# Kernel tuning notes

Measured on AMD Instinct MI355X. Metric: run time of the kernel, lower is better.

## Reference

```python
import jax, jax.numpy as jnp
import numpy as np

B, L, H = 256, 16, 512
D2 = 2 * H  # bidirectional tree-LSTM hidden dim


def setup_inputs() -> dict:
    key = jax.random.key(0)
    ks = jax.random.split(key, 8)
    sc = lambda k, shp, fan: (jax.random.normal(k, shp, jnp.float32) / np.sqrt(fan)).astype(jnp.float32)
    return {
        "idiom_hidden": jax.random.normal(ks[0], (B, L, H), jnp.float32),
        "idiom_length": jax.random.randint(ks[1], (B,), 2, L + 1, jnp.int32),
        "w_ih_f": sc(ks[2], (4 * H, H), H),
        "w_hh_f": sc(ks[3], (4 * H, H), H),
        "b_f": jnp.zeros((4 * H,), jnp.float32),   # b_ih + b_hh fused
        "w_ih_b": sc(ks[4], (4 * H, H), H),
        "w_hh_b": sc(ks[5], (4 * H, H), H),
        "b_b": jnp.zeros((4 * H,), jnp.float32),
        "w_comp": sc(ks[6], (5 * D2, 2 * D2), 2 * D2),
        "b_comp": jnp.zeros((5 * D2,), jnp.float32),
        "w_query": sc(ks[7], (1, D2), D2),
    }


def _lstm(x, w_ih, w_hh, b):
    # x: (B, T, H) -> hs, cs: (B, T, H). PyTorch LSTMCell gate order: i, f, g, o.
    xg = jnp.einsum("bth,gh->btg", x, w_ih) + b  # precompute input gates

    def step(carry, xg_t):
        h, c = carry
        g = xg_t + h @ w_hh.T
        i, f, u, o = jnp.split(g, 4, axis=-1)
        c = jax.nn.sigmoid(f) * c + jax.nn.sigmoid(i) * jnp.tanh(u)
        h = jax.nn.sigmoid(o) * jnp.tanh(c)
        return (h, c), (h, c)

    z = jnp.zeros((x.shape[0], w_hh.shape[1]), x.dtype)
    _, (hs, cs) = jax.lax.scan(step, (z, z), jnp.swapaxes(xg, 0, 1))
    return jnp.swapaxes(hs, 0, 1), jnp.swapaxes(cs, 0, 1)


def _reverse_padded(x, lengths):
    # reverse first `length` positions of each sequence (batch_first)
    T = x.shape[1]
    pos = jnp.arange(T)[None, :]
    ln = lengths[:, None]
    idx = jnp.where(pos < ln, ln - 1 - pos, pos)
    return jnp.take_along_axis(x, idx[:, :, None], axis=1)


def _treelstm(hl, cl, hr, cr, w, b):
    v = jnp.concatenate([hl, hr], axis=-1) @ w.T + b
    i, fl, fr, u, o = jnp.split(v, 5, axis=-1)
    c = cl * jax.nn.sigmoid(fl + 1.0) + cr * jax.nn.sigmoid(fr + 1.0) + jnp.tanh(u) * jax.nn.sigmoid(i)
    h = jax.nn.sigmoid(o) * jnp.tanh(c)
    return h, c


def reference(idiom_hidden, idiom_length, w_ih_f, w_hh_f, b_f, w_ih_b, w_hh_b, b_b, w_comp, b_comp, w_query):
    maxd = idiom_hidden.shape[1]
    lmask = (jnp.arange(maxd)[None, :] < idiom_length[:, None]).astype(idiom_hidden.dtype)

    # bidirectional leaf LSTM
    hs_f, cs_f = _lstm(idiom_hidden, w_ih_f, w_hh_f, b_f)
    x_bw = _reverse_padded(idiom_hidden, idiom_length)
    hs_b, cs_b = _lstm(x_bw, w_ih_b, w_hh_b, b_b)
    hs_b = _reverse_padded(hs_b, idiom_length)
    cs_b = _reverse_padded(cs_b, idiom_length)
    h = jnp.concatenate([hs_f, hs_b], axis=-1)  # (B, L, 2H)
    c = jnp.concatenate([cs_f, cs_b], axis=-1)

    # iterative tree-LSTM composition (shapes shrink by 1 each step -> Python loop over depth)
    for i in range(maxd - 1):
        hl, hr = h[:, :-1, :], h[:, 1:, :]
        cl, cr = c[:, :-1, :], c[:, 1:, :]
        nh, nc = _treelstm(hl, cl, hr, cr, w_comp, b_comp)
        if i < maxd - 2:
            logits = jnp.einsum("bmd,d->bm", nh, w_query[0])
            m = lmask[:, i + 1:]
            masked = logits + (1.0 - m) * -10000.0  # eval-mode greedy_select
            sel = jax.lax.stop_gradient(
                jax.nn.one_hot(jnp.argmax(masked, axis=1), masked.shape[1], dtype=nh.dtype))
            cum = jnp.cumsum(sel, axis=1)
            left = (1.0 - cum)[:, :, None]
            right = (cum - sel)[:, :, None]
            nh = sel[:, :, None] * nh + left * hl + right * hr
            nc = sel[:, :, None] * nc + left * cl + right * cr
        done = lmask[:, i + 1][:, None, None]
        h = done * nh + (1.0 - done) * h[:, :-1, :]
        c = done * nc + (1.0 - done) * c[:, :-1, :]
    # state collapsed to a single node
    return h[:, 0, :]
```

## Files before the change

### kernel.cpp

```cpp
#include <hip/hip_runtime.h>
#include <math.h>

#define NB 256
#define LM 16
#define HID 512
#define H4 2048
#define D2 1024
#define D5 5120
#define NPAIR0 3840
#define INC_CAP 512

typedef __attribute__((ext_vector_type(8))) short bf16x8;
typedef __attribute__((ext_vector_type(4))) float f32x4;

__device__ __forceinline__ float sigm(float x) { return 1.0f / (1.0f + expf(-x)); }

__device__ __forceinline__ unsigned short bf16_rne(float f) {
    union { float f; unsigned u; } v; v.f = f;
    unsigned u = v.u;
    return (unsigned short)((u + 0x7fffu + ((u >> 16) & 1u)) >> 16);
}
__device__ __forceinline__ float bf16_tof(unsigned short h) {
    union { unsigned u; float f; } v; v.u = ((unsigned)h) << 16;
    return v.f;
}

__device__ __forceinline__ void gload16(const unsigned short* g, unsigned short* l) {
    __builtin_amdgcn_global_load_lds(
        (const __attribute__((address_space(1))) void*)(const void*)g,
        (__attribute__((address_space(3))) void*)(void*)l, 16, 0, 0);
}

__global__ __launch_bounds__(256)
void init_kernel(const int* __restrict__ lens, float* ccur,
                 unsigned short* hc_hi, unsigned short* hc_lo,
                 int* pos, int* pair, int4* rowlist0, int4* rowlist_c,
                 int* rcount, float* logits)
{
    int b = blockIdx.x, tid = threadIdx.x;
    for (int u = tid; u < HID; u += 256) {
        ccur[(size_t)b * HID + u] = 0.f;
        ccur[((size_t)NB + b) * HID + u] = 0.f;
        hc_hi[(size_t)b * HID + u] = 0;
        hc_hi[((size_t)NB + b) * HID + u] = 0;
        hc_lo[(size_t)b * HID + u] = 0;
        hc_lo[((size_t)NB + b) * HID + u] = 0;
    }
    if (tid < 16) { pos[b * 16 + tid] = tid; pair[b * 16 + tid] = tid; logits[b * 16 + tid] = -1e30f; }
    if (tid < 15) rowlist0[b * 15 + tid] = make_int4(b, tid, tid + 1, tid | (tid << 16));
    __shared__ int sbase;
    int len = lens[b];
    if (tid == 0) sbase = atomicAdd(rcount + 15, len - 1);
    __syncthreads();
    if (tid < len - 1) rowlist_c[sbase + tid] = make_int4(b, tid, tid + 1, tid | (tid << 16));
}

__global__ __launch_bounds__(256)
void split_w(const float4* __restrict__ w, unsigned short* __restrict__ hi,
             unsigned short* __restrict__ lo, int n4)
{
    for (int i = blockIdx.x * 256 + threadIdx.x; i < n4; i += gridDim.x * 256) {
        float4 f = w[i];
        ushort4 h, l;
        h.x = bf16_rne(f.x); l.x = bf16_rne(f.x - bf16_tof(h.x));
        h.y = bf16_rne(f.y); l.y = bf16_rne(f.y - bf16_tof(h.y));
        h.z = bf16_rne(f.z); l.z = bf16_rne(f.z - bf16_tof(h.z));
        h.w = bf16_rne(f.w); l.w = bf16_rne(f.w - bf16_tof(h.w));
        ((ushort4*)hi)[i] = h;
        ((ushort4*)lo)[i] = l;
    }
}

__global__ __launch_bounds__(256)
void pack_lstm_w(const float* __restrict__ w_ih_f, const float* __restrict__ w_hh_f,
                 const float* __restrict__ w_ih_b, const float* __restrict__ w_hh_b,
                 unsigned short* __restrict__ wl_hi, unsigned short* __restrict__ wl_lo)
{
    const int total4 = 2 * H4 * 256;
    for (int i = blockIdx.x * 256 + threadIdx.x; i < total4; i += gridDim.x * 256) {
        int k4 = i & 255;
        int j = (i >> 8) & 2047;
        int dir = i >> 19;
        const float* wih = dir ? w_ih_b : w_ih_f;
        const float* whh = dir ? w_hh_b : w_hh_f;
        float4 f = (k4 < 128) ? *(const float4*)(wih + (size_t)j * HID + k4 * 4)
                              : *(const float4*)(whh + (size_t)j * HID + (k4 - 128) * 4);
        ushort4 h, l;
        h.x = bf16_rne(f.x); l.x = bf16_rne(f.x - bf16_tof(h.x));
        h.y = bf16_rne(f.y); l.y = bf16_rne(f.y - bf16_tof(h.y));
        h.z = bf16_rne(f.z); l.z = bf16_rne(f.z - bf16_tof(h.z));
        h.w = bf16_rne(f.w); l.w = bf16_rne(f.w - bf16_tof(h.w));
        ((ushort4*)wl_hi)[i] = h;
        ((ushort4*)wl_lo)[i] = l;
    }
}

__global__ __launch_bounds__(256)
void gemm_lstm_g(int t, const int* __restrict__ lens,
                 const unsigned short* __restrict__ x_hi, const unsigned short* __restrict__ x_lo,
                 const unsigned short* __restrict__ hc_hi, const unsigned short* __restrict__ hc_lo,
                 const unsigned short* __restrict__ wl_hi, const unsigned short* __restrict__ wl_lo,
                 float* __restrict__ gbuf)
{
    constexpr int SA = 64 * 32;
    constexpr int SB = 128 * 32;
    constexpr int BUF = 2 * SA + 2 * SB;

    const int row0 = blockIdx.x * 64;
    const int col0 = blockIdx.y * 128;
    const int dir = blockIdx.z & 1;
    const int kz = blockIdx.z >> 1;
    const int kbeg = kz * 512, kend = kbeg + 512;
    float* gout = gbuf + (size_t)kz * 2 * NB * H4;

    const int tid = threadIdx.x, lane = tid & 63, w = tid >> 6;
    const int wm = w >> 1, wn = w & 1;

    __shared__ __align__(16) unsigned short smem[2 * BUF];

    const int sz8 = ((lane & 3) ^ ((lane >> 3) & 3)) * 8;
    const int b0 = row0 + w * 16 + (lane >> 2);
    const int len = lens[b0];
    const int trow = dir ? ((t < len) ? (len - 1 - t) : t) : t;
    const size_t xoff = ((size_t)(b0 * LM + trow)) * HID;
    const size_t hoff = ((size_t)(dir * NB + b0)) * HID;

    size_t colOff[2];
#pragma unroll
    for (int cs = 0; cs < 2; ++cs)
        colOff[cs] = ((size_t)(dir * H4 + col0 + (w + 4 * cs) * 16 + (lane >> 2))) * 1024;

    auto stage = [&](int d, int k) {
        unsigned short* sb = smem + d * BUF;
        const unsigned short* sh = (k < HID) ? (x_hi + xoff + k) : (hc_hi + hoff + (k - HID));
        gload16(sh + sz8, sb + w * 512);
        const unsigned short* sl = (k < HID) ? (x_lo + xoff + k) : (hc_lo + hoff + (k - HID));
        gload16(sl + sz8, sb + SA + w * 512);
#pragma unroll
        for (int j = 0; j < 4; ++j) {
            const int pl = j >> 1, cs = j & 1;
            const unsigned short* wb = pl ? wl_lo : wl_hi;
            gload16(wb + colOff[cs] + k + sz8, sb + 2 * SA + pl * SB + (w + 4 * cs) * 512);
        }
    };

    f32x4 acc[2][4];
#pragma unroll
    for (int i = 0; i < 2; ++i)
#pragma unroll
        for (int j = 0; j < 4; ++j) acc[i][j] = (f32x4){0.f, 0.f, 0.f, 0.f};

    const int rsw = ((lane >> 4) ^ ((lane >> 1) & 3)) * 8;
    const int a_off = (wm * 32 + (lane & 15)) * 32 + rsw;
    const int b_off = 2 * SA + (wn * 64 + (lane & 15)) * 32 + rsw;

    stage(0, kbeg);
    __syncthreads();
    int cur = 0;
    for (int k0 = kbeg; k0 < kend; k0 += 32) {
        if (k0 + 32 < kend) stage(cur ^ 1, k0 + 32);
        const unsigned short* sb = smem + cur * BUF;
        bf16x8 ah[2], al[2];
#pragma unroll
        for (int fm = 0; fm < 2; ++fm) {
            ah[fm] = *(const bf16x8*)&sb[a_off + fm * 512];
            al[fm] = *(const bf16x8*)&sb[SA + a_off + fm * 512];
        }
#pragma unroll
        for (int fn = 0; fn < 4; ++fn) {
            bf16x8 bh = *(const bf16x8*)&sb[b_off + fn * 512];
            bf16x8 bl = *(const bf16x8*)&sb[SB + b_off + fn * 512];
#pragma unroll
            for (int fm = 0; fm < 2; ++fm) {
                acc[fm][fn] = __builtin_amdgcn_mfma_f32_16x16x32_bf16(ah[fm], bh, acc[fm][fn], 0, 0, 0);
                acc[fm][fn] = __builtin_amdgcn_mfma_f32_16x16x32_bf16(ah[fm], bl, acc[fm][fn], 0, 0, 0);
                acc[fm][fn] = __builtin_amdgcn_mfma_f32_16x16x32_bf16(al[fm], bh, acc[fm][fn], 0, 0, 0);
            }
        }
        __syncthreads();
        cur ^= 1;
    }

#pragma unroll
    for (int fm = 0; fm < 2; ++fm) {
        int rbase = row0 + wm * 32 + fm * 16 + (lane >> 4) * 4;
#pragma unroll
        for (int fn = 0; fn < 4; ++fn) {
            int c = col0 + wn * 64 + fn * 16 + (lane & 15);
#pragma unroll
            for (int q = 0; q < 4; ++q)
                gout[((size_t)(dir * NB + rbase + q)) * H4 + c] = acc[fm][fn][q];
        }
    }
}

__global__ __launch_bounds__(256)
void lstm_gate(int t, const int* __restrict__ lengths,
               const float* __restrict__ b_f, const float* __restrict__ b_b,
               const float* __restrict__ g_buf, float* __restrict__ ccur,
               unsigned short* __restrict__ hc_hi, unsigned short* __restrict__ hc_lo,
               unsigned short* __restrict__ h_hi, unsigned short* __restrict__ h_lo,
               float* __restrict__ c_seq)
{
    int b = blockIdx.x, dir = blockIdx.y, tid = threadIdx.x;
    const float* bias = dir ? b_b : b_f;
    int len = lengths[b];
    int pos = dir ? ((t < len) ? (len - 1 - t) : t) : t;
    const float* g0 = g_buf + ((size_t)(dir * NB + b)) * H4;
    const float* g1 = g0 + (size_t)2 * NB * H4;
    float* cc = ccur + ((size_t)(dir * NB + b)) * HID;
    unsigned short* hch = hc_hi + ((size_t)(dir * NB + b)) * HID;
    unsigned short* hcl = hc_lo + ((size_t)(dir * NB + b)) * HID;
    size_t so = ((size_t)(b * LM + pos)) * D2 + dir * HID;
    for (int u = tid; u < HID; u += 256) {
        float gi = g0[u]           + g1[u]           + bias[u];
        float gf = g0[HID + u]     + g1[HID + u]     + bias[HID + u];
        float gu = g0[2 * HID + u] + g1[2 * HID + u] + bias[2 * HID + u];
        float go = g0[3 * HID + u] + g1[3 * HID + u] + bias[3 * HID + u];
        float c = sigm(gf) * cc[u] + sigm(gi) * tanhf(gu);
        float h = sigm(go) * tanhf(c);
        cc[u] = c; c_seq[so + u] = c;
        unsigned short hb = bf16_rne(h);
        unsigned short hl2 = bf16_rne(h - bf16_tof(hb));
        hch[u] = hb; hcl[u] = hl2;
        h_hi[so + u] = hb; h_lo[so + u] = hl2;
    }
}

template<int BM, int KTOT>
__global__ __launch_bounds__(256)
void gemm_pairs_g(const int4* __restrict__ rowlist, int nrows_lit,
                  const int* __restrict__ nrows_ptr, int cap,
                  const unsigned short* __restrict__ h_hi,
                  const unsigned short* __restrict__ h_lo,
                  const unsigned short* __restrict__ w_hi,
                  const unsigned short* __restrict__ w_lo,
                  float* __restrict__ vbuf)
{
    constexpr int WROWS = BM / 2;
    constexpr int FM = WROWS / 16;
    constexpr int NRS = BM / 64;
    constexpr int SA = BM * 32;
    constexpr int SB = 128 * 32;
    constexpr int BUF = 2 * SA + 2 * SB;

    int nrows = nrows_ptr ? *nrows_ptr : nrows_lit;
    const int row0 = blockIdx.x * BM;
    if (row0 >= nrows) return;
    const int col0 = blockIdx.y * 128;
    const int kbeg = blockIdx.z * KTOT;
    const int kend = kbeg + KTOT;
    float* vout = vbuf + (size_t)blockIdx.z * cap * D5;

    const int tid = threadIdx.x, lane = tid & 63, w = tid >> 6;
    const int wm = w >> 1, wn = w & 1;

    __shared__ __align__(16) unsigned short smem[2 * BUF];

    const int sz8 = ((lane & 3) ^ ((lane >> 3) & 3)) * 8;
    size_t offL[NRS], offR[NRS];
#pragma unroll
    for (int rs = 0; rs < NRS; ++rs) {
        int rr = row0 + (w + 4 * rs) * 16 + (lane >> 2);
        if (rr > nrows - 1) rr = nrows - 1;
        int4 e = rowlist[rr];
        if (e.x < 0) { e.x = 0; e.y = 0; e.z = 1; }
        offL[rs] = ((size_t)(e.x * LM + e.y)) * D2;
        offR[rs] = ((size_t)(e.x * LM + e.z)) * D2;
    }
    size_t colOff[2];
#pragma unroll
    for (int cs = 0; cs < 2; ++cs)
        colOff[cs] = ((size_t)(col0 + (w + 4 * cs) * 16 + (lane >> 2))) * H4;

    auto stage = [&](int d, int k) {
        unsigned short* sb = smem + d * BUF;
#pragma unroll
        for (int j = 0; j < 2 * NRS; ++j) {
            const int pl = j / NRS, rs = j % NRS;
            const int g = w + 4 * rs;
            const unsigned short* hb = pl ? h_lo : h_hi;
            size_t off = (k < D2) ? (offL[rs] + k) : (offR[rs] + (k - D2));
            gload16(hb + off + sz8, sb + pl * SA + g * 512);
        }
#pragma unroll
        for (int j = 0; j < 4; ++j) {
            const int pl = j >> 1, cs = j & 1;
            const int g = w + 4 * cs;
            const unsigned short* wb = pl ? w_lo : w_hi;
            gload16(wb + colOff[cs] + k + sz8, sb + 2 * SA + pl * SB + g * 512);
        }
    };

    f32x4 acc[FM][4];
#pragma unroll
    for (int i = 0; i < FM; ++i)
#pragma unroll
        for (int j = 0; j < 4; ++j) acc[i][j] = (f32x4){0.f, 0.f, 0.f, 0.f};

    const int rsw = ((lane >> 4) ^ ((lane >> 1) & 3)) * 8;
    const int a_off = (wm * WROWS + (lane & 15)) * 32 + rsw;
    const int b_off = 2 * SA + (wn * 64 + (lane & 15)) * 32 + rsw;

    stage(0, kbeg);
    __syncthreads();
    int cur = 0;
    for (int k0 = kbeg; k0 < kend; k0 += 32) {
        if (k0 + 32 < kend) stage(cur ^ 1, k0 + 32);
        const unsigned short* sb = smem + cur * BUF;
        bf16x8 ah[FM], al[FM];
#pragma unroll
        for (int fm = 0; fm < FM; ++fm) {
            ah[fm] = *(const bf16x8*)&sb[a_off + fm * 512];
            al[fm] = *(const bf16x8*)&sb[SA + a_off + fm * 512];
        }
#pragma unroll
        for (int fn = 0; fn < 4; ++fn) {
            bf16x8 bh = *(const bf16x8*)&sb[b_off + fn * 512];
            bf16x8 bl = *(const bf16x8*)&sb[SB + b_off + fn * 512];
#pragma unroll
            for (int fm = 0; fm < FM; ++fm) {
                acc[fm][fn] = __builtin_amdgcn_mfma_f32_16x16x32_bf16(ah[fm], bh, acc[fm][fn], 0, 0, 0);
                acc[fm][fn] = __builtin_amdgcn_mfma_f32_16x16x32_bf16(ah[fm], bl, acc[fm][fn], 0, 0, 0);
                acc[fm][fn] = __builtin_amdgcn_mfma_f32_16x16x32_bf16(al[fm], bh, acc[fm][fn], 0, 0, 0);
            }
        }
        __syncthreads();
        cur ^= 1;
    }

#pragma unroll
    for (int fm = 0; fm < FM; ++fm) {
        int rbase = row0 + wm * WROWS + fm * 16 + (lane >> 4) * 4;
#pragma unroll
        for (int fn = 0; fn < 4; ++fn) {
            int c = col0 + wn * 64 + fn * 16 + (lane & 15);
#pragma unroll
            for (int q = 0; q < 4; ++q) {
                int r = rbase + q;
                if (r < nrows) vout[(size_t)r * D5 + c] = acc[fm][fn][q];
            }
        }
    }
}

__device__ __forceinline__ void gates_row(int row, int4 e,
    const float* __restrict__ v_buf, int cap, int nz,
    const float* __restrict__ b_comp, const float* __restrict__ c_seq,
    const float* __restrict__ w_q,
    float* __restrict__ nh_cand, float* __restrict__ nc_cand,
    float* __restrict__ logits)
{
    int b = e.x, sL = e.y, sR = e.z;
    int cslot = e.w & 0xffff, plog = e.w >> 16;
    const float* v = v_buf + (size_t)row * D5;
    const size_t zstride = (size_t)cap * D5;
    const float* cl = c_seq + ((size_t)(b * LM + sL)) * D2;
    const float* cr = c_seq + ((size_t)(b * LM + sR)) * D2;
    float* nh = nh_cand + ((size_t)(b * 15 + cslot)) * D2;
    float* nc = nc_cand + ((size_t)(b * 15 + cslot)) * D2;

    float part = 0.f;
    for (int d = threadIdx.x; d < D2; d += 256) {
        float gi  = v[d];
        float gfl = v[D2 + d];
        float gfr = v[2 * D2 + d];
        float gu  = v[3 * D2 + d];
        float go  = v[4 * D2 + d];
        for (int z = 1; z < nz; ++z) {
            const float* vz = v + z * zstride;
            gi += vz[d]; gfl += vz[D2 + d]; gfr += vz[2 * D2 + d];
            gu += vz[3 * D2 + d]; go += vz[4 * D2 + d];
        }
        gi += b_comp[d]; gfl += b_comp[D2 + d]; gfr += b_comp[2 * D2 + d];
        gu += b_comp[3 * D2 + d]; go += b_comp[4 * D2 + d];
        float c = cl[d] * sigm(gfl + 1.0f) + cr[d] * sigm(gfr + 1.0f) + tanhf(gu) * sigm(gi);
        float h = sigm(go) * tanhf(c);
        nc[d] = c; nh[d] = h;
        part += h * w_q[d];
    }
    for (int o = 32; o > 0; o >>= 1) part += __shfl_down(part, o);
    __shared__ float wsum[4];
    if ((threadIdx.x & 63) == 0) wsum[threadIdx.x >> 6] = part;
    __syncthreads();
    if (threadIdx.x == 0) logits[b * 16 + plog] = wsum[0] + wsum[1] + wsum[2] + wsum[3];
    __syncthreads();
}

__global__ __launch_bounds__(256)
void gates_logits(const int4* __restrict__ rowlist, int nrows_lit,
                  const int* __restrict__ nrows_ptr,
                  const float* __restrict__ v_buf, int cap, int nz,
                  const float* __restrict__ b_comp,
                  const float* __restrict__ c_seq, const float* __restrict__ w_q,
                  float* __restrict__ nh, float* __restrict__ nc,
                  float* __restrict__ logits)
{
    int nrows = nrows_ptr ? *nrows_ptr : nrows_lit;
    int row = blockIdx.x;
    if (row >= nrows) return;
    int4 e = rowlist[row];
    if (e.x < 0) return;
    gates_row(row, e, v_buf, cap, nz, b_comp, c_seq, w_q, nh, nc, logits);
}

__device__ void merge_body(int iter, int b, const int* __restrict__ lengths,
                  float* __restrict__ c_seq,
                  const float* __restrict__ nh_cand, const float* __restrict__ nc_cand,
                  float* __restrict__ logits, int* __restrict__ pos_idx,
                  int* __restrict__ pair_idx, int4* __restrict__ rowlist_out,
                  int* __restrict__ rcount, int4* __restrict__ slotE,
                  int* __restrict__ slotR,
                  unsigned short* __restrict__ h_hi, unsigned short* __restrict__ h_lo)
{
    int tid = threadIdx.x;
    int M = 15 - iter;
    int len = lengths[b];
    bool act = (iter + 1) < len;

    __shared__ float sl[16];
    __shared__ int sp[16], sq[16];
    __shared__ int s_sel;

    if (tid <= M) sp[tid] = pos_idx[b * 16 + tid];
    if (tid < M) { sq[tid] = pair_idx[b * 16 + tid]; sl[tid] = logits[b * 16 + tid]; }
    __syncthreads();

    if (tid == 0) {
        int sel = -1;
        if (act) {
            float best = -INFINITY; sel = 0;
            for (int p2 = 0; p2 < M; ++p2) {
                float mv = ((iter + 1 + p2) < len) ? sl[p2] : (sl[p2] - 10000.0f);
                if (mv > best) { best = mv; sel = p2; }
            }
        }
        s_sel = sel;
    }
    __syncthreads();
    int sel = s_sel;

    if (sel >= 0) {
        int slotL = sp[sel];
        int cslot = sq[sel];
        const float* nh = nh_cand + ((size_t)(b * 15 + cslot)) * D2;
        const float* nc = nc_cand + ((size_t)(b * 15 + cslot)) * D2;
        float* cd = c_seq + ((size_t)(b * LM + slotL)) * D2;
        unsigned short* hh = h_hi + ((size_t)(b * LM + slotL)) * D2;
        unsigned short* hl = h_lo + ((size_t)(b * LM + slotL)) * D2;
        for (int d = tid; d < D2; d += 256) {
            float hv = nh[d];
            cd[d] = nc[d];
            unsigned short hb = bf16_rne(hv);
            hh[d] = hb;
            hl[d] = bf16_rne(hv - bf16_tof(hb));
        }

        if (tid == 0) {
            for (int p2 = sel + 1; p2 < M; ++p2) sp[p2] = sp[p2 + 1];
            for (int p2 = sel + 1; p2 < M - 1; ++p2) { sq[p2] = sq[p2 + 1]; sl[p2] = sl[p2 + 1]; }
            int Mn = M - 1;
            if (iter < 14) {
                int s0 = -1, s1 = -1;
                if (sel - 1 >= 0) {
                    int4 e0 = make_int4(b, sp[sel - 1], sp[sel], sq[sel - 1] | ((sel - 1) << 16));
                    s0 = atomicAdd(rcount, 1);
                    rowlist_out[s0] = e0;
                    slotE[2 * b] = e0;
                }
                if (sel <= Mn - 1) {
                    int4 e1 = make_int4(b, sp[sel], sp[sel + 1], sq[sel] | (sel << 16));
                    s1 = atomicAdd(rcount, 1);
                    rowlist_out[s1] = e1;
                    slotE[2 * b + 1] = e1;
                }
                slotR[2 * b] = s0; slotR[2 * b + 1] = s1;
            }
            for (int p2 = 0; p2 < M; ++p2) pos_idx[b * 16 + p2] = sp[p2];
            for (int p2 = 0; p2 < Mn; ++p2) { pair_idx[b * 16 + p2] = sq[p2]; logits[b * 16 + p2] = sl[p2]; }
        }
    } else {
        if (tid == 0 && iter < 14) { slotR[2 * b] = -1; slotR[2 * b + 1] = -1; }
    }
}

__global__ __launch_bounds__(256)
void merge_kernel(int iter, const int* __restrict__ lens, float* __restrict__ c_seq,
                  const float* __restrict__ nh, const float* __restrict__ nc,
                  float* __restrict__ logits, int* __restrict__ pos, int* __restrict__ pair,
                  int4* __restrict__ rowlist_out, int* __restrict__ rcount,
                  int4* __restrict__ slotE, int* __restrict__ slotR,
                  unsigned short* __restrict__ h_hi, unsigned short* __restrict__ h_lo)
{
    merge_body(iter, blockIdx.x, lens, c_seq, nh, nc, logits, pos, pair,
               rowlist_out, rcount, slotE, slotR, h_hi, h_lo);
}

__global__ __launch_bounds__(256)
void gates_merge(int it, const int* __restrict__ lens,
                 const float* __restrict__ vbuf, int cap, int nz,
                 const float* __restrict__ b_comp, float* __restrict__ c_seq,
                 const float* __restrict__ w_q,
                 float* __restrict__ nh, float* __restrict__ nc,
                 float* __restrict__ logits,
                 int* __restrict__ pos, int* __restrict__ pair,
                 int4* __restrict__ rowlist_out, int* __restrict__ rc_next,
                 int4* __restrict__ slotE, int* __restrict__ slotR,
                 unsigned short* __restrict__ h_hi, unsigned short* __restrict__ h_lo)
{
    int b = blockIdx.x;
    for (int s = 0; s < 2; ++s) {
        int row = slotR[2 * b + s];
        if (row >= 0)
            gates_row(row, slotE[2 * b + s], vbuf, cap, nz, b_comp, c_seq, w_q, nh, nc, logits);
        __syncthreads();
    }
    merge_body(it + 1, b, lens, c_seq, nh, nc, logits, pos, pair,
               rowlist_out, rc_next, slotE, slotR, h_hi, h_lo);
}

__global__ __launch_bounds__(256)
void copy_out(const unsigned short* __restrict__ h_hi,
              const unsigned short* __restrict__ h_lo, float* __restrict__ out)
{
    int b = blockIdx.x;
    size_t base = (size_t)(b * LM) * D2;
    for (int d = threadIdx.x; d < D2; d += 256)
        out[(size_t)b * D2 + d] = bf16_tof(h_hi[base + d]) + bf16_tof(h_lo[base + d]);
}

extern "C" void kernel_launch(void* const* d_in, const int* in_sizes, int n_in,
                              void* d_out, int out_size, void* d_ws, size_t ws_size,
                              hipStream_t stream)
{
    const float* x      = (const float*)d_in[0];
    const int*   lens   = (const int*)  d_in[1];
    const float* w_ih_f = (const float*)d_in[2];
    const float* w_hh_f = (const float*)d_in[3];
    const float* b_f    = (const float*)d_in[4];
    const float* w_ih_b = (const float*)d_in[5];
    const float* w_hh_b = (const float*)d_in[6];
    const float* b_b    = (const float*)d_in[7];
    const float* w_comp = (const float*)d_in[8];
    const float* b_comp = (const float*)d_in[9];
    const float* w_q    = (const float*)d_in[10];
    float* out = (float*)d_out;

    char* p = (char*)d_ws;
    auto alloc = [&](size_t bytes) {
        char* q = p; p += (bytes + 255) & ~(size_t)255; return q;
    };
    float* c_seq = (float*)alloc((size_t)NB * LM * D2 * 4);
    float* nh    = (float*)alloc((size_t)NB * 15 * D2 * 4);
    float* nc    = (float*)alloc((size_t)NB * 15 * D2 * 4);
    unsigned short* h_hi = (unsigned short*)alloc((size_t)NB * LM * D2 * 2);
    unsigned short* h_lo = (unsigned short*)alloc((size_t)NB * LM * D2 * 2);
    unsigned short* w_hi = (unsigned short*)alloc((size_t)D5 * H4 * 2);
    unsigned short* w_lo = (unsigned short*)alloc((size_t)D5 * H4 * 2);
    unsigned short* x_hi = (unsigned short*)alloc((size_t)NB * LM * HID * 2);
    unsigned short* x_lo = (unsigned short*)alloc((size_t)NB * LM * HID * 2);
    unsigned short* wl_hi = (unsigned short*)alloc((size_t)2 * H4 * 1024 * 2);
    unsigned short* wl_lo = (unsigned short*)alloc((size_t)2 * H4 * 1024 * 2);
    unsigned short* hc_hi = (unsigned short*)alloc((size_t)2 * NB * HID * 2);
    unsigned short* hc_lo = (unsigned short*)alloc((size_t)2 * NB * HID * 2);
    float* ccur  = (float*)alloc((size_t)2 * NB * HID * 4);
    float* logits = (float*)alloc((size_t)NB * 16 * 4);
    int*   pos    = (int*)alloc((size_t)NB * 16 * 4);
    int*   pair   = (int*)alloc((size_t)NB * 16 * 4);
    int4*  rowlist0   = (int4*)alloc((size_t)NPAIR0 * 16);
    int4*  rowlist_c  = (int4*)alloc((size_t)NPAIR0 * 16);
    int4*  rowlist_inc= (int4*)alloc((size_t)INC_CAP * 16);
    int4*  slotE  = (int4*)alloc((size_t)2 * NB * 16);
    int*   slotR  = (int*)alloc((size_t)2 * NB * 4);
    int*   rcount = (int*)alloc(16 * 4);
    char* tail = p;
    float* gbuf = (float*)tail;
    float* vbuf = (float*)tail;

    size_t used = (size_t)(tail - (char*)d_ws);
    size_t avail = (ws_size > used) ? (ws_size - used) : 0;
    size_t maxc = avail / ((size_t)D5 * 4);
    if (maxc > (size_t)NPAIR0) maxc = NPAIR0;
    int chunk = ((int)maxc) & ~127;
    if (chunk < 2048) chunk = 2048;

    hipMemsetAsync(rcount, 0, 64, stream);
    init_kernel<<<dim3(NB), dim3(256), 0, stream>>>(lens, ccur, hc_hi, hc_lo, pos, pair,
                                                    rowlist0, rowlist_c, rcount, logits);
    split_w<<<dim3(2048), dim3(256), 0, stream>>>((const float4*)w_comp, w_hi, w_lo, (int)((size_t)D5 * H4 / 4));
    split_w<<<dim3(1024), dim3(256), 0, stream>>>((const float4*)x, x_hi, x_lo, (int)((size_t)NB * LM * HID / 4));
    pack_lstm_w<<<dim3(1024), dim3(256), 0, stream>>>(w_ih_f, w_hh_f, w_ih_b, w_hh_b, wl_hi, wl_lo);

    for (int t = 0; t < 16; ++t) {
        gemm_lstm_g<<<dim3(4, 16, 4), dim3(256), 0, stream>>>(
            t, lens, x_hi, x_lo, hc_hi, hc_lo, wl_hi, wl_lo, gbuf);
        lstm_gate<<<dim3(NB, 2), dim3(256), 0, stream>>>(
            t, lens, b_f, b_b, gbuf, ccur, hc_hi, hc_lo, h_hi, h_lo, c_seq);
    }

    if (chunk >= NPAIR0) {
        gemm_pairs_g<128, 2048><<<dim3(30, 40, 1), dim3(256), 0, stream>>>(
            rowlist_c, NPAIR0, (const int*)(rcount + 15), 0,
            h_hi, h_lo, w_hi, w_lo, vbuf);
        gates_logits<<<dim3(NPAIR0), dim3(256), 0, stream>>>(
            rowlist_c, NPAIR0, (const int*)(rcount + 15),
            vbuf, 0, 1, b_comp, c_seq, w_q, nh, nc, logits);
    } else {
        for (int off = 0; off < NPAIR0; off += chunk) {
            int rows = NPAIR0 - off; if (rows > chunk) rows = chunk;
            int RT = (rows + 127) >> 7;
            gemm_pairs_g<128, 2048><<<dim3(RT, 40, 1), dim3(256), 0, stream>>>(
                rowlist0 + off, rows, (const int*)nullptr, 0,
                h_hi, h_lo, w_hi, w_lo, vbuf);
            gates_logits<<<dim3(rows), dim3(256), 0, stream>>>(
                rowlist0 + off, rows, (const int*)nullptr,
                vbuf, 0, 1, b_comp, c_seq, w_q, nh, nc, logits);
        }
    }

    merge_kernel<<<dim3(NB), dim3(256), 0, stream>>>(
        0, lens, c_seq, nh, nc, logits, pos, pair,
        rowlist_inc, rcount + 0, slotE, slotR, h_hi, h_lo);
    for (int it = 0; it < 14; ++it) {
        gemm_pairs_g<128, 512><<<dim3(4, 40, 4), dim3(256), 0, stream>>>(
            rowlist_inc, 0, (const int*)(rcount + it), INC_CAP,
            h_hi, h_lo, w_hi, w_lo, vbuf);
        gates_merge<<<dim3(NB), dim3(256), 0, stream>>>(
            it, lens, vbuf, INC_CAP, 4, b_comp, c_seq, w_q, nh, nc, logits,
            pos, pair, rowlist_inc, rcount + it + 1, slotE, slotR, h_hi, h_lo);
    }

    copy_out<<<dim3(NB), dim3(256), 0, stream>>>(h_hi, h_lo, out);
}
```

Baseline: 1.470 ms.

## Swizzle GEMM block indices for XCD locality and parallelize merge gate slots

The LSTM and incremental pair GEMMs now use a flattened 1D grid. Block IDs are remapped so the four row tiles that share a weight column tile land on the same XCD, likely a mod-8 round-robin guess, which should improve L2 reuse of the weight slices. gates_merge now handles its two candidate slots at the same time with 128 threads each, instead of processing them one after another with block-wide syncs, and writes the logits through a small shared reduction. This reduces serialization per iteration, but it depends on the hardware's block-to-XCD dispatch order.

Result: faster. 1.369 ms (-6.9%).

```diff
diff --git a/kernel.cpp b/kernel.cpp
--- a/kernel.cpp
+++ b/kernel.cpp
@@ -106,10 +106,15 @@
     constexpr int SB = 128 * 32;
     constexpr int BUF = 2 * SA + 2 * SB;
 
-    const int row0 = blockIdx.x * 64;
-    const int col0 = blockIdx.y * 128;
-    const int dir = blockIdx.z & 1;
-    const int kz = blockIdx.z >> 1;
+    const int bid = blockIdx.x;
+    const int x8 = bid & 7, r = bid >> 3;
+    const int sub = r & 3, gq = r >> 2;
+    const int g = x8 + 8 * gq;
+    const int row0 = sub * 64;
+    const int col0 = (g & 15) * 128;
+    const int zz = g >> 4;
+    const int dir = zz & 1;
+    const int kz = zz >> 1;
     const int kbeg = kz * 512, kend = kbeg + 512;
     float* gout = gbuf + (size_t)kz * 2 * NB * H4;
 
@@ -227,7 +232,7 @@
     }
 }
 
-template<int BM, int KTOT>
+template<int BM, int KTOT, bool SWZ>
 __global__ __launch_bounds__(256)
 void gemm_pairs_g(const int4* __restrict__ rowlist, int nrows_lit,
                   const int* __restrict__ nrows_ptr, int cap,
@@ -245,12 +250,24 @@
     constexpr int BUF = 2 * SA + 2 * SB;
 
     int nrows = nrows_ptr ? *nrows_ptr : nrows_lit;
-    const int row0 = blockIdx.x * BM;
+
+    int sub, yc, kz;
+    if constexpr (SWZ) {
+        const int bid = blockIdx.x;
+        const int x8 = bid & 7, r = bid >> 3;
+        sub = r & 3;
+        const int g = x8 + 8 * (r >> 2);
+        yc = g % 40; kz = g / 40;
+    } else {
+        sub = blockIdx.x; yc = blockIdx.y; kz = blockIdx.z;
+    }
+
+    const int row0 = sub * BM;
     if (row0 >= nrows) return;
-    const int col0 = blockIdx.y * 128;
-    const int kbeg = blockIdx.z * KTOT;
+    const int col0 = yc * 128;
+    const int kbeg = kz * KTOT;
     const int kend = kbeg + KTOT;
-    float* vout = vbuf + (size_t)blockIdx.z * cap * D5;
+    float* vout = vbuf + (size_t)kz * cap * D5;
 
     const int tid = threadIdx.x, lane = tid & 63, w = tid >> 6;
     const int wm = w >> 1, wn = w & 1;
@@ -278,17 +295,17 @@
 #pragma unroll
         for (int j = 0; j < 2 * NRS; ++j) {
             const int pl = j / NRS, rs = j % NRS;
-            const int g = w + 4 * rs;
+            const int g2 = w + 4 * rs;
             const unsigned short* hb = pl ? h_lo : h_hi;
             size_t off = (k < D2) ? (offL[rs] + k) : (offR[rs] + (k - D2));
-            gload16(hb + off + sz8, sb + pl * SA + g * 512);
+            gload16(hb + off + sz8, sb + pl * SA + g2 * 512);
         }
 #pragma unroll
         for (int j = 0; j < 4; ++j) {
             const int pl = j >> 1, cs = j & 1;
-            const int g = w + 4 * cs;
+            const int g2 = w + 4 * cs;
             const unsigned short* wb = pl ? w_lo : w_hi;
-            gload16(wb + colOff[cs] + k + sz8, sb + 2 * SA + pl * SB + g * 512);
+            gload16(wb + colOff[cs] + k + sz8, sb + 2 * SA + pl * SB + g2 * 512);
         }
     };
 
@@ -337,8 +354,8 @@
             int c = col0 + wn * 64 + fn * 16 + (lane & 15);
 #pragma unroll
             for (int q = 0; q < 4; ++q) {
-                int r = rbase + q;
-                if (r < nrows) vout[(size_t)r * D5 + c] = acc[fm][fn][q];
+                int r2 = rbase + q;
+                if (r2 < nrows) vout[(size_t)r2 * D5 + c] = acc[fm][fn][q];
             }
         }
     }
@@ -501,7 +518,7 @@
                  const float* __restrict__ vbuf, int cap, int nz,
                  const float* __restrict__ b_comp, float* __restrict__ c_seq,
                  const float* __restrict__ w_q,
-                 float* __restrict__ nh, float* __restrict__ nc,
+                 float* __restrict__ nh_cand, float* __restrict__ nc_cand,
                  float* __restrict__ logits,
                  int* __restrict__ pos, int* __restrict__ pair,
                  int4* __restrict__ rowlist_out, int* __restrict__ rc_next,
@@ -509,13 +526,51 @@
                  unsigned short* __restrict__ h_hi, unsigned short* __restrict__ h_lo)
 {
     int b = blockIdx.x;
-    for (int s = 0; s < 2; ++s) {
-        int row = slotR[2 * b + s];
-        if (row >= 0)
-            gates_row(row, slotE[2 * b + s], vbuf, cap, nz, b_comp, c_seq, w_q, nh, nc, logits);
-        __syncthreads();
-    }
-    merge_body(it + 1, b, lens, c_seq, nh, nc, logits, pos, pair,
+    int tid = threadIdx.x;
+    int slot = tid >> 7, tid2 = tid & 127;
+    int row = slotR[2 * b + slot];
+    int4 e = slotE[2 * b + slot];
+
+    __shared__ float wsum2[2][2];
+
+    float part = 0.f;
+    if (row >= 0) {
+        int cslot = e.w & 0xffff;
+        const float* v = vbuf + (size_t)row * D5;
+        const size_t zstride = (size_t)cap * D5;
+        const float* cl = c_seq + ((size_t)(b * LM + e.y)) * D2;
+        const float* cr = c_seq + ((size_t)(b * LM + e.z)) * D2;
+        float* nh = nh_cand + ((size_t)(b * 15 + cslot)) * D2;
+        float* nc = nc_cand + ((size_t)(b * 15 + cslot)) * D2;
+        for (int d = tid2; d < D2; d += 128) {
+            float gi  = v[d];
+            float gfl = v[D2 + d];
+            float gfr = v[2 * D2 + d];
+            float gu  = v[3 * D2 + d];
+            float go  = v[4 * D2 + d];
+            for (int z = 1; z < nz; ++z) {
+                const float* vz = v + z * zstride;
+                gi += vz[d]; gfl += vz[D2 + d]; gfr += vz[2 * D2 + d];
+                gu += vz[3 * D2 + d]; go += vz[4 * D2 + d];
+            }
+            gi += b_comp[d]; gfl += b_comp[D2 + d]; gfr += b_comp[2 * D2 + d];
+            gu += b_comp[3 * D2 + d]; go += b_comp[4 * D2 + d];
+            float c = cl[d] * sigm(gfl + 1.0f) + cr[d] * sigm(gfr + 1.0f) + tanhf(gu) * sigm(gi);
+            float h = sigm(go) * tanhf(c);
+            nc[d] = c; nh[d] = h;
+            part += h * w_q[d];
+        }
+    }
+    for (int o = 32; o > 0; o >>= 1) part += __shfl_down(part, o);
+    if ((tid2 & 63) == 0) wsum2[slot][tid2 >> 6] = part;
+    __syncthreads();
+    if (row >= 0 && tid2 == 0) {
+        int plog = e.w >> 16;
+        logits[b * 16 + plog] = wsum2[slot][0] + wsum2[slot][1];
+    }
+    __syncthreads();
+
+    merge_body(it + 1, b, lens, c_seq, nh_cand, nc_cand, logits, pos, pair,
                rowlist_out, rc_next, slotE, slotR, h_hi, h_lo);
 }
 
@@ -592,14 +647,14 @@
     pack_lstm_w<<<dim3(1024), dim3(256), 0, stream>>>(w_ih_f, w_hh_f, w_ih_b, w_hh_b, wl_hi, wl_lo);
 
     for (int t = 0; t < 16; ++t) {
-        gemm_lstm_g<<<dim3(4, 16, 4), dim3(256), 0, stream>>>(
+        gemm_lstm_g<<<dim3(256), dim3(256), 0, stream>>>(
             t, lens, x_hi, x_lo, hc_hi, hc_lo, wl_hi, wl_lo, gbuf);
         lstm_gate<<<dim3(NB, 2), dim3(256), 0, stream>>>(
             t, lens, b_f, b_b, gbuf, ccur, hc_hi, hc_lo, h_hi, h_lo, c_seq);
     }
 
     if (chunk >= NPAIR0) {
-        gemm_pairs_g<128, 2048><<<dim3(30, 40, 1), dim3(256), 0, stream>>>(
+        gemm_pairs_g<128, 2048, false><<<dim3(30, 40, 1), dim3(256), 0, stream>>>(
             rowlist_c, NPAIR0, (const int*)(rcount + 15), 0,
             h_hi, h_lo, w_hi, w_lo, vbuf);
         gates_logits<<<dim3(NPAIR0), dim3(256), 0, stream>>>(
@@ -609,7 +664,7 @@
         for (int off = 0; off < NPAIR0; off += chunk) {
             int rows = NPAIR0 - off; if (rows > chunk) rows = chunk;
             int RT = (rows + 127) >> 7;
-            gemm_pairs_g<128, 2048><<<dim3(RT, 40, 1), dim3(256), 0, stream>>>(
+            gemm_pairs_g<128, 2048, false><<<dim3(RT, 40, 1), dim3(256), 0, stream>>>(
                 rowlist0 + off, rows, (const int*)nullptr, 0,
                 h_hi, h_lo, w_hi, w_lo, vbuf);
             gates_logits<<<dim3(rows), dim3(256), 0, stream>>>(
@@ -622,7 +677,7 @@
         0, lens, c_seq, nh, nc, logits, pos, pair,
         rowlist_inc, rcount + 0, slotE, slotR, h_hi, h_lo);
     for (int it = 0; it < 14; ++it) {
-        gemm_pairs_g<128, 512><<<dim3(4, 40, 4), dim3(256), 0, stream>>>(
+        gemm_pairs_g<128, 512, true><<<dim3(640), dim3(256), 0, stream>>>(
             rowlist_inc, 0, (const int*)(rcount + it), INC_CAP,
             h_hi, h_lo, w_hi, w_lo, vbuf);
         gates_merge<<<dim3(NB), dim3(256), 0, stream>>>(
```
